# Performance work log

Hardware: AMD Instinct MI355X
Metric: run time of the kernel (lower is better)

The kernel has to match this reference:

```python
import jax, jax.numpy as jnp
from jax import lax
import numpy as np


def setup_inputs() -> dict:
    key = jax.random.key(0)
    k1, k2 = jax.random.split(key)
    inputs = jax.random.normal(k1, (32, 64, 64, 128), dtype=jnp.float32)
    # glorot-like scale for a 3x3x128->256 kernel
    kernel = jax.random.normal(k2, (3, 3, 128, 256), dtype=jnp.float32) * 0.03
    return {"inputs": inputs, "kernel": kernel}


def reference(inputs, kernel):
    # Stride-1 VALID conv, NHWC inputs, HWIO kernel (same math as the unrolled
    # per-pixel patch*kernel + reduce_sum loop in conv2d_manual).
    conv = lax.conv_general_dilated(
        inputs, kernel,
        window_strides=(1, 1), padding="VALID",
        dimension_numbers=("NHWC", "HWIO", "NHWC"),
    )  # [B, OH, OW, F]
    B, OH, OW, F = conv.shape
    # Faithfully replicate the original TensorArray stack (OH*OW, B, F)
    # followed by a raw reshape to (B, OH, OW, F) (element-permuting).
    stacked = jnp.moveaxis(conv, 0, 2)            # (OH, OW, B, F)
    out = stacked.reshape(B, OH, OW, F)           # raw reshape, as in original
    return jax.nn.relu(out)
```

## Files before the change

kernel.cpp:

```cpp
#include <hip/hip_runtime.h>

typedef short bf16x8 __attribute__((ext_vector_type(8)));
typedef float f32x4 __attribute__((ext_vector_type(4)));
typedef unsigned short u16;

__device__ __forceinline__ u16 f2bf(float f) {
    unsigned u = __builtin_bit_cast(unsigned, f);
    u += 0x7FFF + ((u >> 16) & 1);
    return (u16)(u >> 16);
}

constexpr int Hh = 64, Ww = 64, Ci = 128;
constexpr int Fo = 256, OH = 62, OW = 62;
constexpr int Ktot = 3 * 3 * Ci;
constexpr int BM = 128, BK = 64;
constexpr int NSTEP = Ktot / BK;
constexpr int NWG = 1922;
constexpr long NEL_IN = 32L * 64 * 64 * 128;
constexpr size_t WS_IN_BYTES = (size_t)NEL_IN * 2;
constexpr size_t WS_WT_OFF   = WS_IN_BYTES;
constexpr size_t WS_NEED     = WS_IN_BYTES + 294912ull * 2;

#define GLD_LDS(src, dst) __builtin_amdgcn_global_load_lds( \
    (const __attribute__((address_space(1))) unsigned int*)(src), \
    (__attribute__((address_space(3))) unsigned int*)(dst), 16, 0, 0)

__global__ __launch_bounds__(256) void cvt_input(const float* __restrict__ in,
                                                 u16* __restrict__ ob) {
    const int i = blockIdx.x * 256 + threadIdx.x;
    const float4* s = (const float4*)in + (long)i * 2;
    float4 v0 = s[0], v1 = s[1];
    bf16x8 p;
    p[0] = (short)f2bf(v0.x); p[1] = (short)f2bf(v0.y);
    p[2] = (short)f2bf(v0.z); p[3] = (short)f2bf(v0.w);
    p[4] = (short)f2bf(v1.x); p[5] = (short)f2bf(v1.y);
    p[6] = (short)f2bf(v1.z); p[7] = (short)f2bf(v1.w);
    ((bf16x8*)ob)[i] = p;
}

__global__ __launch_bounds__(256) void cvt_wt(const float* __restrict__ wt,
                                              u16* __restrict__ ob) {
    const int t = blockIdx.x * 256 + threadIdx.x;
    const int f = t / 144, k8 = t % 144;
    bf16x8 p;
    #pragma unroll
    for (int j = 0; j < 8; ++j)
        p[j] = (short)f2bf(wt[(k8 * 8 + j) * Fo + f]);
    ((bf16x8*)ob)[f * 144 + k8] = p;
}

__global__ __launch_bounds__(256) void conv_mfma(
    const u16* __restrict__ inb,
    const u16* __restrict__ wtb,
    float* __restrict__ out)
{
    __shared__ __align__(16) short As[2][BM * BK];
    __shared__ __align__(16) short Bs[2][BM * BK];

    const int tid  = threadIdx.x;
    const int lane = tid & 63;
    const int wv   = tid >> 6;
    const int wr   = wv >> 1, wc = wv & 1;

    constexpr int q = NWG / 8, rr = NWG % 8;
    const int orig = blockIdx.x;
    const int xcd = orig & 7, idx = orig >> 3;
    const int wgid = (xcd < rr ? xcd * (q + 1) : rr * (q + 1) + (xcd - rr) * q) + idx;

    const int colb = wgid & 1;
    const int rowb = wgid >> 1;
    const int r0   = rowb * BM;
    const int f0g  = colb * 128;

    const int lrow8 = lane >> 3;
    const int schunk = ((lane & 7) ^ lrow8) * 16;
    long abyte[4], bbyte[4];
    #pragma unroll
    for (int j = 0; j < 4; ++j) {
        const int r  = r0 + wv * 32 + j * 8 + lrow8;
        const int bb = r & 31;
        const int pix = r >> 5;
        const int ow = pix % OW, oh = pix / OW;
        abyte[j] = (long)(((bb * Hh + oh) * Ww + ow) * Ci) * 2 + schunk;
        const int f = f0g + wv * 32 + j * 8 + lrow8;
        bbyte[j] = (long)f * (Ktot * 2) + schunk;
    }

    auto stage = [&](int step, int buf) {
        const int kb = step >> 1, c0 = (step & 1) << 6;
        const int kh = kb / 3, kw = kb % 3;
        const long tap = (long)((kh * Ww + kw) * Ci + c0) * 2;
        const long bof = (long)step * 128;
        #pragma unroll
        for (int j = 0; j < 4; ++j)
            GLD_LDS((const char*)inb + abyte[j] + tap, &As[buf][(wv * 32 + j * 8) * BK]);
        #pragma unroll
        for (int j = 0; j < 4; ++j)
            GLD_LDS((const char*)wtb + bbyte[j] + bof, &Bs[buf][(wv * 32 + j * 8) * BK]);
    };

    f32x4 acc[4][4];
    #pragma unroll
    for (int m = 0; m < 4; ++m)
        #pragma unroll
        for (int n = 0; n < 4; ++n) acc[m][n] = (f32x4){0.f, 0.f, 0.f, 0.f};

    stage(0, 0);
    __syncthreads();

    const int lrow = lane & 15;
    const int lq   = lane >> 4;

    for (int step = 0; step < NSTEP; ++step) {
        const int cur = step & 1;
        if (step + 1 < NSTEP) stage(step + 1, cur ^ 1);

        #pragma unroll
        for (int ks = 0; ks < 2; ++ks) {
            bf16x8 a[4], b[4];
            const int off = ks * 64 + lq * 16;
            #pragma unroll
            for (int m = 0; m < 4; ++m) {
                const int row = wr * 64 + m * 16 + lrow;
                a[m] = *(const bf16x8*)((const char*)As[cur] + row * 128 + (off ^ ((row & 7) << 4)));
            }
            #pragma unroll
            for (int n = 0; n < 4; ++n) {
                const int row = wc * 64 + n * 16 + lrow;
                b[n] = *(const bf16x8*)((const char*)Bs[cur] + row * 128 + (off ^ ((row & 7) << 4)));
            }
            __builtin_amdgcn_s_setprio(1);
            #pragma unroll
            for (int m = 0; m < 4; ++m)
                #pragma unroll
                for (int n = 0; n < 4; ++n)
                    acc[m][n] = __builtin_amdgcn_mfma_f32_16x16x32_bf16(a[m], b[n], acc[m][n], 0, 0, 0);
            __builtin_amdgcn_s_setprio(0);
        }
        __syncthreads();
    }

    const int lcol = lane & 15;
    const int lr4  = (lane >> 4) * 4;
    #pragma unroll
    for (int m = 0; m < 4; ++m) {
        #pragma unroll
        for (int n = 0; n < 4; ++n) {
            const int col = f0g + wc * 64 + n * 16 + lcol;
            const int rowbase = r0 + wr * 64 + m * 16 + lr4;
            #pragma unroll
            for (int e = 0; e < 4; ++e) {
                float v = acc[m][n][e];
                out[(rowbase + e) * Fo + col] = v > 0.f ? v : 0.f;
            }
        }
    }
}

__global__ __launch_bounds__(256) void conv_mfma_fb(
    const float* __restrict__ in, const float* __restrict__ wt,
    float* __restrict__ out)
{
    __shared__ __align__(16) short As[BM * BK];
    __shared__ __align__(16) short Bs[BM * BK];
    const int tid  = threadIdx.x;
    const int lane = tid & 63;
    const int wv   = tid >> 6;
    const int wr   = wv >> 1, wc = wv & 1;
    constexpr int q = NWG / 8, rr = NWG % 8;
    const int orig = blockIdx.x;
    const int xcd = orig & 7, idx = orig >> 3;
    const int wgid = (xcd < rr ? xcd * (q + 1) : rr * (q + 1) + (xcd - rr) * q) + idx;
    const int colb = wgid & 1;
    const int rowb = wgid >> 1;
    const int r0   = rowb * BM;
    const int f0g  = colb * 128;
    const int ai = tid >> 1;
    const int ah = tid & 1;
    const int r  = r0 + ai;
    const int bb  = r & 31;
    const int pix = r >> 5;
    const int ow  = pix % OW;
    const int oh  = pix / OW;
    const float* abase = in + ((bb * Hh + oh) * Ww + ow) * Ci;
    const int bk = tid & 63;
    const int bf = (tid >> 6) * 32;

    auto loadA = [&](int step, float4 (&pa)[8]) {
        const int kb = step >> 1;
        const int c0 = (step & 1) << 6;
        const int kh = kb / 3, kw = kb % 3;
        const float* src = abase + (kh * Ww + kw) * Ci + c0 + ah * 32;
        #pragma unroll
        for (int c = 0; c < 8; ++c) pa[c] = ((const float4*)src)[c];
    };
    auto writeA = [&](const float4 (&pa)[8]) {
        char* dst = (char*)As + ai * 128;
        const int swz = (ai & 7) << 4;
        #pragma unroll
        for (int c = 0; c < 4; ++c) {
            float4 v0 = pa[2 * c], v1 = pa[2 * c + 1];
            bf16x8 p;
            p[0] = (short)f2bf(v0.x); p[1] = (short)f2bf(v0.y);
            p[2] = (short)f2bf(v0.z); p[3] = (short)f2bf(v0.w);
            p[4] = (short)f2bf(v1.x); p[5] = (short)f2bf(v1.y);
            p[6] = (short)f2bf(v1.z); p[7] = (short)f2bf(v1.w);
            *(bf16x8*)(dst + ((ah * 64 + c * 16) ^ swz)) = p;
        }
    };
    auto loadB = [&](int step, float4 (&pb)[8]) {
        const float* src = wt + (step * BK + bk) * Fo + f0g + bf;
        #pragma unroll
        for (int c = 0; c < 8; ++c) pb[c] = ((const float4*)src)[c];
    };
    auto writeB = [&](const float4 (&pb)[8]) {
        const int k2 = bk * 2;
        #pragma unroll
        for (int c = 0; c < 8; ++c) {
            float4 v = pb[c];
            const int fl = bf + c * 4;
            *(u16*)((char*)Bs + (fl + 0) * 128 + (k2 ^ (((fl + 0) & 7) << 4))) = f2bf(v.x);
            *(u16*)((char*)Bs + (fl + 1) * 128 + (k2 ^ (((fl + 1) & 7) << 4))) = f2bf(v.y);
            *(u16*)((char*)Bs + (fl + 2) * 128 + (k2 ^ (((fl + 2) & 7) << 4))) = f2bf(v.z);
            *(u16*)((char*)Bs + (fl + 3) * 128 + (k2 ^ (((fl + 3) & 7) << 4))) = f2bf(v.w);
        }
    };

    f32x4 acc[4][4];
    #pragma unroll
    for (int m = 0; m < 4; ++m)
        #pragma unroll
        for (int n = 0; n < 4; ++n) acc[m][n] = (f32x4){0.f, 0.f, 0.f, 0.f};
    {
        float4 pa[8], pb[8];
        loadA(0, pa); loadB(0, pb);
        writeA(pa); writeB(pb);
    }
    __syncthreads();
    const int lrow = lane & 15;
    const int lq   = lane >> 4;
    for (int step = 0; step < NSTEP; ++step) {
        float4 na[8], nb[8];
        if (step + 1 < NSTEP) { loadA(step + 1, na); loadB(step + 1, nb); }
        #pragma unroll
        for (int ks = 0; ks < 2; ++ks) {
            bf16x8 a[4], b[4];
            const int off = ks * 64 + lq * 16;
            #pragma unroll
            for (int m = 0; m < 4; ++m) {
                const int row = wr * 64 + m * 16 + lrow;
                a[m] = *(const bf16x8*)((const char*)As + row * 128 + (off ^ ((row & 7) << 4)));
            }
            #pragma unroll
            for (int n = 0; n < 4; ++n) {
                const int row = wc * 64 + n * 16 + lrow;
                b[n] = *(const bf16x8*)((const char*)Bs + row * 128 + (off ^ ((row & 7) << 4)));
            }
            #pragma unroll
            for (int m = 0; m < 4; ++m)
                #pragma unroll
                for (int n = 0; n < 4; ++n)
                    acc[m][n] = __builtin_amdgcn_mfma_f32_16x16x32_bf16(a[m], b[n], acc[m][n], 0, 0, 0);
        }
        __syncthreads();
        if (step + 1 < NSTEP) { writeA(na); writeB(nb); }
        __syncthreads();
    }
    const int lcol = lane & 15;
    const int lr4  = (lane >> 4) * 4;
    #pragma unroll
    for (int m = 0; m < 4; ++m) {
        #pragma unroll
        for (int n = 0; n < 4; ++n) {
            const int col = f0g + wc * 64 + n * 16 + lcol;
            const int rowbase = r0 + wr * 64 + m * 16 + lr4;
            #pragma unroll
            for (int e = 0; e < 4; ++e) {
                float v = acc[m][n][e];
                out[(rowbase + e) * Fo + col] = v > 0.f ? v : 0.f;
            }
        }
    }
}

extern "C" void kernel_launch(void* const* d_in, const int* in_sizes, int n_in,
                              void* d_out, int out_size, void* d_ws, size_t ws_size,
                              hipStream_t stream) {
    const float* in  = (const float*)d_in[0];
    const float* wt  = (const float*)d_in[1];
    float* out = (float*)d_out;
    if (ws_size >= WS_NEED) {
        u16* inb = (u16*)d_ws;
        u16* wtb = (u16*)((char*)d_ws + WS_WT_OFF);
        cvt_input<<<dim3(8192), dim3(256), 0, stream>>>(in, inb);
        cvt_wt<<<dim3(144), dim3(256), 0, stream>>>(wt, wtb);
        conv_mfma<<<dim3(NWG), dim3(256), 0, stream>>>(inb, wtb, out);
    } else {
        conv_mfma_fb<<<dim3(NWG), dim3(256), 0, stream>>>(in, wt, out);
    }
}
```

Before: 114.5 us.

## Widen conv tile to full 256 filters with 8 waves and triple-buffered LDS

The main conv kernel now covers all 256 output filters per workgroup (128x256 tile, 512 threads, 8 waves), which halves the number of workgroups and removes the duplicate A-tile loads that came from splitting filters across two blocks. The double-buffered LDS pipeline becomes a three-stage ring with explicit vmcnt waits and raw barriers, so global-to-LDS loads run two steps ahead of compute. The cost is a larger LDS footprint (about 144KB per block), which limits occupancy to one block per CU and leaves fewer blocks for load balancing across CUs.

```diff
diff --git a/kernel.cpp b/kernel.cpp
--- a/kernel.cpp
+++ b/kernel.cpp
@@ -13,9 +13,9 @@
 constexpr int Hh = 64, Ww = 64, Ci = 128;
 constexpr int Fo = 256, OH = 62, OW = 62;
 constexpr int Ktot = 3 * 3 * Ci;
-constexpr int BM = 128, BK = 64;
+constexpr int BM = 128, BN = 256, BK = 64;
 constexpr int NSTEP = Ktot / BK;
-constexpr int NWG = 1922;
+constexpr int NWG = 961;
 constexpr long NEL_IN = 32L * 64 * 64 * 128;
 constexpr size_t WS_IN_BYTES = (size_t)NEL_IN * 2;
 constexpr size_t WS_WT_OFF   = WS_IN_BYTES;
@@ -24,6 +24,7 @@
 #define GLD_LDS(src, dst) __builtin_amdgcn_global_load_lds( \
     (const __attribute__((address_space(1))) unsigned int*)(src), \
     (__attribute__((address_space(3))) unsigned int*)(dst), 16, 0, 0)
+#define MEMFENCE asm volatile("" ::: "memory")
 
 __global__ __launch_bounds__(256) void cvt_input(const float* __restrict__ in,
                                                  u16* __restrict__ ob) {
@@ -49,54 +50,53 @@
     ((bf16x8*)ob)[f * 144 + k8] = p;
 }
 
-__global__ __launch_bounds__(256) void conv_mfma(
+__global__ __launch_bounds__(512) void conv_mfma(
     const u16* __restrict__ inb,
     const u16* __restrict__ wtb,
     float* __restrict__ out)
 {
-    __shared__ __align__(16) short As[2][BM * BK];
-    __shared__ __align__(16) short Bs[2][BM * BK];
+    __shared__ __align__(16) short As[3][BM * BK];
+    __shared__ __align__(16) short Bs[3][BN * BK];
 
     const int tid  = threadIdx.x;
     const int lane = tid & 63;
     const int wv   = tid >> 6;
-    const int wr   = wv >> 1, wc = wv & 1;
+    const int wr   = wv >> 2, wc = wv & 3;
 
     constexpr int q = NWG / 8, rr = NWG % 8;
     const int orig = blockIdx.x;
     const int xcd = orig & 7, idx = orig >> 3;
     const int wgid = (xcd < rr ? xcd * (q + 1) : rr * (q + 1) + (xcd - rr) * q) + idx;
-
-    const int colb = wgid & 1;
-    const int rowb = wgid >> 1;
-    const int r0   = rowb * BM;
-    const int f0g  = colb * 128;
+    const int r0 = wgid * BM;
 
     const int lrow8 = lane >> 3;
     const int schunk = ((lane & 7) ^ lrow8) * 16;
-    long abyte[4], bbyte[4];
-    #pragma unroll
-    for (int j = 0; j < 4; ++j) {
-        const int r  = r0 + wv * 32 + j * 8 + lrow8;
+    long abyte[2], bbyte[4];
+    #pragma unroll
+    for (int j = 0; j < 2; ++j) {
+        const int r  = r0 + wv * 16 + j * 8 + lrow8;
         const int bb = r & 31;
         const int pix = r >> 5;
         const int ow = pix % OW, oh = pix / OW;
         abyte[j] = (long)(((bb * Hh + oh) * Ww + ow) * Ci) * 2 + schunk;
-        const int f = f0g + wv * 32 + j * 8 + lrow8;
+    }
+    #pragma unroll
+    for (int j = 0; j < 4; ++j) {
+        const int f = wv * 32 + j * 8 + lrow8;
         bbyte[j] = (long)f * (Ktot * 2) + schunk;
     }
 
-    auto stage = [&](int step, int buf) {
+    auto stage = [&](int step, int p) {
         const int kb = step >> 1, c0 = (step & 1) << 6;
         const int kh = kb / 3, kw = kb % 3;
         const long tap = (long)((kh * Ww + kw) * Ci + c0) * 2;
         const long bof = (long)step * 128;
         #pragma unroll
+        for (int j = 0; j < 2; ++j)
+            GLD_LDS((const char*)inb + abyte[j] + tap, &As[p][(wv * 16 + j * 8) * BK]);
+        #pragma unroll
         for (int j = 0; j < 4; ++j)
-            GLD_LDS((const char*)inb + abyte[j] + tap, &As[buf][(wv * 32 + j * 8) * BK]);
-        #pragma unroll
-        for (int j = 0; j < 4; ++j)
-            GLD_LDS((const char*)wtb + bbyte[j] + bof, &Bs[buf][(wv * 32 + j * 8) * BK]);
+            GLD_LDS((const char*)wtb + bbyte[j] + bof, &Bs[p][(wv * 32 + j * 8) * BK]);
     };
 
     f32x4 acc[4][4];
@@ -105,16 +105,18 @@
         #pragma unroll
         for (int n = 0; n < 4; ++n) acc[m][n] = (f32x4){0.f, 0.f, 0.f, 0.f};
 
-    stage(0, 0);
-    __syncthreads();
+    stage(0, 0); stage(1, 1); stage(2, 2);
+    asm volatile("s_waitcnt vmcnt(12)" ::: "memory");
+    __builtin_amdgcn_s_barrier();
+    MEMFENCE;
 
     const int lrow = lane & 15;
     const int lq   = lane >> 4;
 
+    int p = 0;
     for (int step = 0; step < NSTEP; ++step) {
-        const int cur = step & 1;
-        if (step + 1 < NSTEP) stage(step + 1, cur ^ 1);
-
+        const char* Ab = (const char*)&As[p][0];
+        const char* Bb = (const char*)&Bs[p][0];
         #pragma unroll
         for (int ks = 0; ks < 2; ++ks) {
             bf16x8 a[4], b[4];
@@ -122,12 +124,12 @@
             #pragma unroll
             for (int m = 0; m < 4; ++m) {
                 const int row = wr * 64 + m * 16 + lrow;
-                a[m] = *(const bf16x8*)((const char*)As[cur] + row * 128 + (off ^ ((row & 7) << 4)));
+                a[m] = *(const bf16x8*)(Ab + row * 128 + (off ^ ((row & 7) << 4)));
             }
             #pragma unroll
             for (int n = 0; n < 4; ++n) {
-                const int row = wc * 64 + n * 16 + lrow;
-                b[n] = *(const bf16x8*)((const char*)Bs[cur] + row * 128 + (off ^ ((row & 7) << 4)));
+                const int f = wc * 64 + n * 16 + lrow;
+                b[n] = *(const bf16x8*)(Bb + f * 128 + (off ^ ((f & 7) << 4)));
             }
             __builtin_amdgcn_s_setprio(1);
             #pragma unroll
@@ -137,7 +139,22 @@
                     acc[m][n] = __builtin_amdgcn_mfma_f32_16x16x32_bf16(a[m], b[n], acc[m][n], 0, 0, 0);
             __builtin_amdgcn_s_setprio(0);
         }
-        __syncthreads();
+        if (step == NSTEP - 1) break;
+
+        MEMFENCE;
+        __builtin_amdgcn_s_barrier();
+        MEMFENCE;
+        if (step + 3 < NSTEP) {
+            stage(step + 3, p);
+            asm volatile("s_waitcnt vmcnt(12)" ::: "memory");
+        } else if (step + 3 == NSTEP) {
+            asm volatile("s_waitcnt vmcnt(6)" ::: "memory");
+        } else {
+            asm volatile("s_waitcnt vmcnt(0)" ::: "memory");
+        }
+        __builtin_amdgcn_s_barrier();
+        MEMFENCE;
+        p = (p == 2) ? 0 : p + 1;
     }
 
     const int lcol = lane & 15;
@@ -146,12 +163,12 @@
     for (int m = 0; m < 4; ++m) {
         #pragma unroll
         for (int n = 0; n < 4; ++n) {
-            const int col = f0g + wc * 64 + n * 16 + lcol;
+            const int col = wc * 64 + n * 16 + lcol;
             const int rowbase = r0 + wr * 64 + m * 16 + lr4;
             #pragma unroll
             for (int e = 0; e < 4; ++e) {
                 float v = acc[m][n][e];
-                out[(rowbase + e) * Fo + col] = v > 0.f ? v : 0.f;
+                out[(long)(rowbase + e) * Fo + col] = v > 0.f ? v : 0.f;
             }
         }
     }
@@ -161,19 +178,20 @@
     const float* __restrict__ in, const float* __restrict__ wt,
     float* __restrict__ out)
 {
-    __shared__ __align__(16) short As[BM * BK];
-    __shared__ __align__(16) short Bs[BM * BK];
+    __shared__ __align__(16) short As[128 * BK];
+    __shared__ __align__(16) short Bs[128 * BK];
     const int tid  = threadIdx.x;
     const int lane = tid & 63;
     const int wv   = tid >> 6;
     const int wr   = wv >> 1, wc = wv & 1;
-    constexpr int q = NWG / 8, rr = NWG % 8;
+    constexpr int NWG2 = 1922;
+    constexpr int q2 = NWG2 / 8, rr2 = NWG2 % 8;
     const int orig = blockIdx.x;
     const int xcd = orig & 7, idx = orig >> 3;
-    const int wgid = (xcd < rr ? xcd * (q + 1) : rr * (q + 1) + (xcd - rr) * q) + idx;
+    const int wgid = (xcd < rr2 ? xcd * (q2 + 1) : rr2 * (q2 + 1) + (xcd - rr2) * q2) + idx;
     const int colb = wgid & 1;
     const int rowb = wgid >> 1;
-    const int r0   = rowb * BM;
+    const int r0   = rowb * 128;
     const int f0g  = colb * 128;
     const int ai = tid >> 1;
     const int ah = tid & 1;
@@ -200,12 +218,12 @@
         #pragma unroll
         for (int c = 0; c < 4; ++c) {
             float4 v0 = pa[2 * c], v1 = pa[2 * c + 1];
-            bf16x8 p;
-            p[0] = (short)f2bf(v0.x); p[1] = (short)f2bf(v0.y);
-            p[2] = (short)f2bf(v0.z); p[3] = (short)f2bf(v0.w);
-            p[4] = (short)f2bf(v1.x); p[5] = (short)f2bf(v1.y);
-            p[6] = (short)f2bf(v1.z); p[7] = (short)f2bf(v1.w);
-            *(bf16x8*)(dst + ((ah * 64 + c * 16) ^ swz)) = p;
+            bf16x8 pk;
+            pk[0] = (short)f2bf(v0.x); pk[1] = (short)f2bf(v0.y);
+            pk[2] = (short)f2bf(v0.z); pk[3] = (short)f2bf(v0.w);
+            pk[4] = (short)f2bf(v1.x); pk[5] = (short)f2bf(v1.y);
+            pk[6] = (short)f2bf(v1.z); pk[7] = (short)f2bf(v1.w);
+            *(bf16x8*)(dst + ((ah * 64 + c * 16) ^ swz)) = pk;
         }
     };
     auto loadB = [&](int step, float4 (&pb)[8]) {
@@ -294,8 +312,8 @@
         u16* wtb = (u16*)((char*)d_ws + WS_WT_OFF);
         cvt_input<<<dim3(8192), dim3(256), 0, stream>>>(in, inb);
         cvt_wt<<<dim3(144), dim3(256), 0, stream>>>(wt, wtb);
-        conv_mfma<<<dim3(NWG), dim3(256), 0, stream>>>(inb, wtb, out);
+        conv_mfma<<<dim3(NWG), dim3(512), 0, stream>>>(inb, wtb, out);
     } else {
-        conv_mfma_fb<<<dim3(NWG), dim3(256), 0, stream>>>(in, wt, out);
-    }
-}
+        conv_mfma_fb<<<dim3(1922), dim3(256), 0, stream>>>(in, wt, out);
+    }
+}
```

Result: slower. 129.3 us (+12.9%).
